# Optimization experiments

Hardware: AMD Instinct MI355X
Metric: run time of the kernel (lower is better)

## Reference

```python
import jax, jax.numpy as jnp
import numpy as np

C = 128
N, H, W = 4, 256, 256
BN_EPS = 1e-5


def _conv(x, w, b=None, groups=1):
    # x: [N,C,H,W], w: [O, I/groups, kh, kw]
    y = jax.lax.conv_general_dilated(
        x, w, window_strides=(1, 1), padding='SAME',
        dimension_numbers=('NCHW', 'OIHW', 'NCHW'),
        feature_group_count=groups)
    if b is not None:
        y = y + b[None, :, None, None]
    return y


def _bn(x, g, b, m, v):
    # eval-mode batchnorm with running stats
    inv = g / jnp.sqrt(v + BN_EPS)
    return x * inv[None, :, None, None] + (b - m * inv)[None, :, None, None]


def _patches3x3(x):
    # [N,C,H,W] -> [N,C,9,H,W], row-major kernel order (matches F.unfold)
    n, c, h, w = x.shape
    xp = jnp.pad(x, ((0, 0), (0, 0), (1, 1), (1, 1)))
    return jnp.stack([xp[:, :, i:i + h, j:j + w]
                      for i in range(3) for j in range(3)], axis=2)


def setup_inputs() -> dict:
    key = jax.random.key(0)
    ks = jax.random.split(key, 16)
    d = {}
    d['coef'] = jax.random.normal(ks[0], (N, C, H, W), jnp.float32)
    d['ms'] = jax.random.normal(ks[1], (N, C, H, W), jnp.float32)
    # fix_weight: depthwise 3x3, no bias + BN
    d['fix_w'] = jax.random.normal(ks[2], (C, 1, 3, 3), jnp.float32) * 0.1
    d['bn1_g'] = 1.0 + 0.1 * jax.random.normal(ks[3], (C,), jnp.float32)
    d['bn1_b'] = 0.1 * jax.random.normal(ks[4], (C,), jnp.float32)
    d['bn1_m'] = 0.1 * jax.random.normal(ks[5], (C,), jnp.float32)
    d['bn1_v'] = 0.5 + jax.random.uniform(ks[6], (C,), jnp.float32)
    # dyn_weight: Conv2d(C, 9, 3, pad 1)
    d['dyn_w'] = jax.random.normal(ks[7], (9, C, 3, 3), jnp.float32) * 0.05
    d['dyn_b'] = 0.05 * jax.random.normal(ks[8], (9,), jnp.float32)
    # dyn_tail BN
    d['bn2_g'] = 1.0 + 0.1 * jax.random.normal(ks[9], (C,), jnp.float32)
    d['bn2_b'] = 0.1 * jax.random.normal(ks[10], (C,), jnp.float32)
    d['bn2_m'] = 0.1 * jax.random.normal(ks[11], (C,), jnp.float32)
    d['bn2_v'] = 0.5 + jax.random.uniform(ks[12], (C,), jnp.float32)
    # refine 1x1: 2C -> C
    d['refine_w'] = jax.random.normal(ks[13], (C, 2 * C, 1, 1), jnp.float32) * 0.05
    d['refine_b'] = 0.05 * jax.random.normal(ks[14], (C,), jnp.float32)
    # SSModule joint_prob_head 3x3: C -> C
    d['joint_w'] = jax.random.normal(ks[15], (C, C, 3, 3), jnp.float32) * 0.03
    d['joint_b'] = 0.03 * jax.random.normal(jax.random.fold_in(key, 99), (C,), jnp.float32)
    return d


def reference(coef, ms, fix_w, bn1_g, bn1_b, bn1_m, bn1_v,
              dyn_w, dyn_b, bn2_g, bn2_b, bn2_m, bn2_v,
              refine_w, refine_b, joint_w, joint_b):
    # fix branch: depthwise conv + BN + ReLU
    fix_ms = jax.nn.relu(_bn(_conv(ms, fix_w, groups=C), bn1_g, bn1_b, bn1_m, bn1_v))
    # dynamic per-pixel kernel: [N,9,H,W], L1-normalized over kernel taps
    dyn_kernel = _conv(ms, dyn_w, dyn_b)
    dyn_kernel = dyn_kernel / jnp.sum(jnp.abs(dyn_kernel), axis=1, keepdims=True)
    # unfold + einsum: spatially-varying depthwise 3x3 conv
    patches = _patches3x3(ms)                                  # [N,C,9,H,W]
    dyn_ms = jnp.einsum('nkhw,nckhw->nchw', dyn_kernel, patches)
    dyn_ms = jax.nn.relu(_bn(dyn_ms, bn2_g, bn2_b, bn2_m, bn2_v))
    # concat + 1x1 refine
    fused = _conv(jnp.concatenate([dyn_ms, fix_ms], axis=1), refine_w, refine_b)
    # SSModule gating
    p = coef + fused
    p2 = jax.nn.sigmoid(_conv(p, joint_w, joint_b))
    return (1.0 - p2) * fused + p2 * coef
```

## Files before the change

kernel.cpp:

```cpp
#include <hip/hip_runtime.h>
#include <hip/hip_bf16.h>
#include <math.h>

#define N_ 4
#define C_ 128
#define H_ 256
#define W_ 256
#define HW_ (H_*W_)
#define BN_EPS 1e-5f

typedef __attribute__((ext_vector_type(8))) short bf16x8;
typedef __attribute__((ext_vector_type(4))) float floatx4;

__device__ __forceinline__ short f2bf(float v) {
    __hip_bfloat16 h = __float2bfloat16(v);
    return __builtin_bit_cast(short, h);
}

__global__ __launch_bounds__(256) void k_prep(const float* __restrict__ refine_w,
                                              const float* __restrict__ joint_w,
                                              short* __restrict__ rwf,
                                              short* __restrict__ jwf) {
    int i = blockIdx.x * 256 + threadIdx.x;
    if (i < 32768) {
        int j      = i & 7;
        int lane   = (i >> 3) & 63;
        int cotile = (i >> 9) & 7;
        int cic    = (i >> 12) & 7;
        int co = cotile * 16 + (lane & 15);
        int ii = cic * 32 + (lane >> 4) * 8 + j;
        rwf[i] = f2bf(refine_w[co * 256 + ii]);
    }
    if (i < 147456) {
        int j      = i & 7;
        int lane   = (i >> 3) & 63;
        int cotile = (i >> 9) & 7;
        int cic    = (i >> 12) & 3;
        int t      = i >> 14;
        int co = cotile * 16 + (lane & 15);
        int ci = cic * 32 + (lane >> 4) * 8 + j;
        jwf[i] = f2bf(joint_w[(co * 128 + ci) * 9 + t]);
    }
}

__global__ __launch_bounds__(256) void k_dyn(const float* __restrict__ ms,
                                             const float* __restrict__ dyn_w,
                                             const float* __restrict__ dyn_b,
                                             float* __restrict__ dk) {
    __shared__ float ms_s[8 * 18 * 18];
    int tid = threadIdx.x;
    int tx = tid & 15, ty = tid >> 4;
    int n = blockIdx.z;
    int h0 = blockIdx.y * 16, w0 = blockIdx.x * 16;
    float acc[9];
#pragma unroll
    for (int k = 0; k < 9; k++) acc[k] = dyn_b[k];

    for (int cc = 0; cc < 16; cc++) {
        __syncthreads();
        for (int e = tid; e < 8 * 18 * 18; e += 256) {
            int ch = e / 324, r = (e % 324) / 18, cl = e % 18;
            int gh = h0 + r - 1, gw = w0 + cl - 1;
            float v = 0.f;
            if (gh >= 0 && gh < H_ && gw >= 0 && gw < W_)
                v = ms[(size_t)(n * C_ + cc * 8 + ch) * HW_ + gh * W_ + gw];
            ms_s[e] = v;
        }
        __syncthreads();
        for (int c8 = 0; c8 < 8; c8++) {
            int c = cc * 8 + c8;
            float m[9];
#pragma unroll
            for (int dy = 0; dy < 3; dy++)
#pragma unroll
                for (int dx = 0; dx < 3; dx++)
                    m[dy * 3 + dx] = ms_s[c8 * 324 + (ty + dy) * 18 + tx + dx];
#pragma unroll
            for (int k = 0; k < 9; k++) {
#pragma unroll
                for (int t = 0; t < 9; t++)
                    acc[k] += m[t] * dyn_w[(k * C_ + c) * 9 + t];
            }
        }
    }
    float s = 0.f;
#pragma unroll
    for (int k = 0; k < 9; k++) s += fabsf(acc[k]);
    float inv = 1.f / s;
    int h = h0 + ty, w = w0 + tx;
#pragma unroll
    for (int k = 0; k < 9; k++)
        dk[(size_t)(n * 9 + k) * HW_ + h * W_ + w] = acc[k] * inv;
}

#define AIP 264
__global__ __launch_bounds__(256) void k_fused(const float* __restrict__ ms,
                                               const float* __restrict__ dk,
                                               const float* __restrict__ fix_w,
                                               const float* __restrict__ bn1_g,
                                               const float* __restrict__ bn1_b,
                                               const float* __restrict__ bn1_m,
                                               const float* __restrict__ bn1_v,
                                               const float* __restrict__ bn2_g,
                                               const float* __restrict__ bn2_b,
                                               const float* __restrict__ bn2_m,
                                               const float* __restrict__ bn2_v,
                                               const short* __restrict__ rwf,
                                               const float* __restrict__ refine_b,
                                               float* __restrict__ fused) {
    __shared__ short act_s[64 * AIP];
    __shared__ float ms_s[8 * 100];
    __shared__ float dk_s[9 * 64];
    int tid = threadIdx.x;
    int n = blockIdx.z;
    int h0 = blockIdx.y * 8, w0 = blockIdx.x * 8;

    for (int e = tid; e < 9 * 64; e += 256) {
        int t = e >> 6, px = e & 63;
        dk_s[e] = dk[(size_t)(n * 9 + t) * HW_ + (h0 + (px >> 3)) * W_ + (w0 + (px & 7))];
    }

    int c8 = tid & 7;
    int pxh = tid >> 3;

    for (int cc = 0; cc < 16; cc++) {
        __syncthreads();
        for (int e = tid; e < 800; e += 256) {
            int ch = e / 100, r = (e % 100) / 10, cl = e % 10;
            int gh = h0 + r - 1, gw = w0 + cl - 1;
            float v = 0.f;
            if (gh >= 0 && gh < H_ && gw >= 0 && gw < W_)
                v = ms[(size_t)(n * C_ + cc * 8 + ch) * HW_ + gh * W_ + gw];
            ms_s[e] = v;
        }
        __syncthreads();
        int c = cc * 8 + c8;
        float i1 = bn1_g[c] * rsqrtf(bn1_v[c] + BN_EPS);
        float b1 = bn1_b[c] - bn1_m[c] * i1;
        float i2 = bn2_g[c] * rsqrtf(bn2_v[c] + BN_EPS);
        float b2 = bn2_b[c] - bn2_m[c] * i2;
        float fw[9];
#pragma unroll
        for (int t = 0; t < 9; t++) fw[t] = fix_w[c * 9 + t];
#pragma unroll
        for (int it = 0; it < 2; it++) {
            int px = pxh + it * 32;
            int py = px >> 3, pxx = px & 7;
            float m[9];
#pragma unroll
            for (int dy = 0; dy < 3; dy++)
#pragma unroll
                for (int dx = 0; dx < 3; dx++)
                    m[dy * 3 + dx] = ms_s[c8 * 100 + (py + dy) * 10 + pxx + dx];
            float dyn = 0.f, fix = 0.f;
#pragma unroll
            for (int t = 0; t < 9; t++) {
                dyn += m[t] * dk_s[t * 64 + px];
                fix += m[t] * fw[t];
            }
            dyn = fmaxf(dyn * i2 + b2, 0.f);
            fix = fmaxf(fix * i1 + b1, 0.f);
            act_s[px * AIP + c] = f2bf(dyn);
            act_s[px * AIP + 128 + c] = f2bf(fix);
        }
    }
    __syncthreads();

    int lane = tid & 63;
    int wave = __builtin_amdgcn_readfirstlane(tid >> 6);
    int cl16 = lane & 15;
    int q = lane >> 4;
    int pxb = wave * 16;

    floatx4 acc[8];
#pragma unroll
    for (int ct = 0; ct < 8; ct++) acc[ct] = (floatx4){0.f, 0.f, 0.f, 0.f};

    const bf16x8* rwv = (const bf16x8*)rwf;
#pragma unroll
    for (int cic = 0; cic < 8; cic++) {
        bf16x8 B = *(const bf16x8*)(act_s + (pxb + cl16) * AIP + q * 8 + cic * 32);
        const bf16x8* Ap = rwv + cic * 8 * 64 + lane;
        bf16x8 A[8];
#pragma unroll
        for (int ct = 0; ct < 8; ct++) A[ct] = Ap[ct * 64];
#pragma unroll
        for (int ct = 0; ct < 8; ct++)
            acc[ct] = __builtin_amdgcn_mfma_f32_16x16x32_bf16(A[ct], B, acc[ct], 0, 0, 0);
    }

    int px = pxb + cl16;
    int h = h0 + (px >> 3), w = w0 + (px & 7);
#pragma unroll
    for (int ct = 0; ct < 8; ct++) {
#pragma unroll
        for (int r = 0; r < 4; r++) {
            int co = ct * 16 + q * 4 + r;
            fused[(size_t)(n * C_ + co) * HW_ + h * W_ + w] = acc[ct][r] + refine_b[co];
        }
    }
}

#define CIP 136
__global__ __launch_bounds__(256, 3) void k_out(const float* __restrict__ coef,
                                                const float* __restrict__ fused,
                                                const short* __restrict__ jwf,
                                                const float* __restrict__ joint_b,
                                                float* __restrict__ out) {
    __shared__ short p_s[180 * CIP];
    int tid = threadIdx.x;
    int n = blockIdx.z;
    int h0 = blockIdx.y * 8, w0 = blockIdx.x * 16;

    for (int it = 0; it < 90; it++) {
        int e = tid + it * 256;
        int ci = e / 180, sp = e - ci * 180;
        int row = sp / 18, col = sp - row * 18;
        int gh = h0 + row - 1, gw = w0 + col - 1;
        float v = 0.f;
        if (gh >= 0 && gh < H_ && gw >= 0 && gw < W_) {
            size_t idx = (size_t)(n * C_ + ci) * HW_ + gh * W_ + gw;
            v = coef[idx] + fused[idx];
        }
        p_s[sp * CIP + ci] = f2bf(v);
    }
    __syncthreads();

    int lane = tid & 63;
    int wave = __builtin_amdgcn_readfirstlane(tid >> 6);
    int c = lane & 15;
    int q = lane >> 4;
    int py0 = wave;
    int py1 = wave + 4;

    floatx4 acc[8][2];
#pragma unroll
    for (int ct = 0; ct < 8; ct++)
#pragma unroll
        for (int p = 0; p < 2; p++)
            acc[ct][p] = (floatx4){0.f, 0.f, 0.f, 0.f};

    const bf16x8* jwv = (const bf16x8*)jwf;

    for (int t = 0; t < 9; t++) {
        int dy = t / 3, dx = t - dy * 3;
        int sb0 = ((py0 + dy) * 18 + c + dx) * CIP + q * 8;
        int sb1 = ((py1 + dy) * 18 + c + dx) * CIP + q * 8;
#pragma unroll
        for (int cic = 0; cic < 4; cic++) {
            bf16x8 B0 = *(const bf16x8*)(p_s + sb0 + cic * 32);
            bf16x8 B1 = *(const bf16x8*)(p_s + sb1 + cic * 32);
            const bf16x8* Ap = jwv + ((t * 4 + cic) * 8) * 64 + lane;
            bf16x8 A[8];
#pragma unroll
            for (int ct = 0; ct < 8; ct++) A[ct] = Ap[ct * 64];
#pragma unroll
            for (int ct = 0; ct < 8; ct++) {
                acc[ct][0] = __builtin_amdgcn_mfma_f32_16x16x32_bf16(A[ct], B0, acc[ct][0], 0, 0, 0);
                acc[ct][1] = __builtin_amdgcn_mfma_f32_16x16x32_bf16(A[ct], B1, acc[ct][1], 0, 0, 0);
            }
        }
    }

    int w = w0 + c;
#pragma unroll
    for (int ct = 0; ct < 8; ct++) {
#pragma unroll
        for (int p = 0; p < 2; p++) {
            int h = h0 + (p == 0 ? py0 : py1);
#pragma unroll
            for (int r = 0; r < 4; r++) {
                int co = ct * 16 + q * 4 + r;
                size_t idx = (size_t)(n * C_ + co) * HW_ + h * W_ + w;
                float z = acc[ct][p][r] + joint_b[co];
                float p2 = 1.f / (1.f + __expf(-z));
                float f = fused[idx], cf = coef[idx];
                out[idx] = f + p2 * (cf - f);
            }
        }
    }
}

extern "C" void kernel_launch(void* const* d_in, const int* in_sizes, int n_in,
                              void* d_out, int out_size, void* d_ws, size_t ws_size,
                              hipStream_t stream) {
    const float* coef     = (const float*)d_in[0];
    const float* ms       = (const float*)d_in[1];
    const float* fix_w    = (const float*)d_in[2];
    const float* bn1_g    = (const float*)d_in[3];
    const float* bn1_b    = (const float*)d_in[4];
    const float* bn1_m    = (const float*)d_in[5];
    const float* bn1_v    = (const float*)d_in[6];
    const float* dyn_w    = (const float*)d_in[7];
    const float* dyn_b    = (const float*)d_in[8];
    const float* bn2_g    = (const float*)d_in[9];
    const float* bn2_b    = (const float*)d_in[10];
    const float* bn2_m    = (const float*)d_in[11];
    const float* bn2_v    = (const float*)d_in[12];
    const float* refine_w = (const float*)d_in[13];
    const float* refine_b = (const float*)d_in[14];
    const float* joint_w  = (const float*)d_in[15];
    const float* joint_b  = (const float*)d_in[16];
    float* out = (float*)d_out;

    float* ws    = (float*)d_ws;
    float* fused = ws;
    float* dk    = fused + (size_t)N_ * C_ * HW_;
    short* jwf   = (short*)(dk + (size_t)N_ * 9 * HW_);
    short* rwf   = jwf + 147456;

    dim3 blk(256);
    k_prep<<<dim3(576), blk, 0, stream>>>(refine_w, joint_w, rwf, jwf);
    k_dyn<<<dim3(16, 16, 4), blk, 0, stream>>>(ms, dyn_w, dyn_b, dk);
    k_fused<<<dim3(32, 32, 4), blk, 0, stream>>>(ms, dk, fix_w,
                                                 bn1_g, bn1_b, bn1_m, bn1_v,
                                                 bn2_g, bn2_b, bn2_m, bn2_v,
                                                 rwf, refine_b, fused);
    k_out<<<dim3(16, 32, 4), blk, 0, stream>>>(coef, fused, jwf, joint_b, out);
}
```

Baseline: 1.068 ms.

## Store fused and gate input as channel-last bf16 to cut k_out traffic

k_fused now writes fused and p = coef + fused as bf16 in an NHWC layout, replacing the fp32 NCHW fused buffer. The sum that k_out used to build in its staging loop now happens earlier, in k_fused. k_out loads the halo tile with 16-byte vector loads straight into LDS, dropping the strided per-channel coef+fused gathers and the per-element conversions. This lowers intermediate memory traffic, but rounding fused to bf16 adds error in the final blend, and k_fused must now also read coef.

```diff
diff --git a/kernel.cpp b/kernel.cpp
--- a/kernel.cpp
+++ b/kernel.cpp
@@ -15,6 +15,10 @@
 __device__ __forceinline__ short f2bf(float v) {
     __hip_bfloat16 h = __float2bfloat16(v);
     return __builtin_bit_cast(short, h);
+}
+__device__ __forceinline__ float bf2f(short s) {
+    unsigned u = ((unsigned)(unsigned short)s) << 16;
+    return __builtin_bit_cast(float, u);
 }
 
 __global__ __launch_bounds__(256) void k_prep(const float* __restrict__ refine_w,
@@ -96,6 +100,7 @@
 #define AIP 264
 __global__ __launch_bounds__(256) void k_fused(const float* __restrict__ ms,
                                                const float* __restrict__ dk,
+                                               const float* __restrict__ coef,
                                                const float* __restrict__ fix_w,
                                                const float* __restrict__ bn1_g,
                                                const float* __restrict__ bn1_b,
@@ -107,7 +112,8 @@
                                                const float* __restrict__ bn2_v,
                                                const short* __restrict__ rwf,
                                                const float* __restrict__ refine_b,
-                                               float* __restrict__ fused) {
+                                               short* __restrict__ fusedbf,
+                                               short* __restrict__ pbf) {
     __shared__ short act_s[64 * AIP];
     __shared__ float ms_s[8 * 100];
     __shared__ float dk_s[9 * 64];
@@ -191,19 +197,31 @@
 
     int px = pxb + cl16;
     int h = h0 + (px >> 3), w = w0 + (px & 7);
+    size_t spi = ((size_t)(n * H_) + h) * W_ + w;
 #pragma unroll
     for (int ct = 0; ct < 8; ct++) {
-#pragma unroll
-        for (int r = 0; r < 4; r++) {
-            int co = ct * 16 + q * 4 + r;
-            fused[(size_t)(n * C_ + co) * HW_ + h * W_ + w] = acc[ct][r] + refine_b[co];
-        }
+        int co0 = ct * 16 + q * 4;
+        float cf[4];
+#pragma unroll
+        for (int r = 0; r < 4; r++)
+            cf[r] = coef[(size_t)(n * C_ + co0 + r) * HW_ + h * W_ + w];
+        short4 fb, pb;
+        float f0 = acc[ct][0] + refine_b[co0 + 0];
+        float f1 = acc[ct][1] + refine_b[co0 + 1];
+        float f2_ = acc[ct][2] + refine_b[co0 + 2];
+        float f3 = acc[ct][3] + refine_b[co0 + 3];
+        fb.x = f2bf(f0);  fb.y = f2bf(f1);  fb.z = f2bf(f2_);  fb.w = f2bf(f3);
+        pb.x = f2bf(f0 + cf[0]); pb.y = f2bf(f1 + cf[1]);
+        pb.z = f2bf(f2_ + cf[2]); pb.w = f2bf(f3 + cf[3]);
+        *(short4*)(fusedbf + spi * 128 + co0) = fb;
+        *(short4*)(pbf + spi * 128 + co0) = pb;
     }
 }
 
 #define CIP 136
 __global__ __launch_bounds__(256, 3) void k_out(const float* __restrict__ coef,
-                                                const float* __restrict__ fused,
+                                                const short* __restrict__ fusedbf,
+                                                const short* __restrict__ pbf,
                                                 const short* __restrict__ jwf,
                                                 const float* __restrict__ joint_b,
                                                 float* __restrict__ out) {
@@ -212,17 +230,18 @@
     int n = blockIdx.z;
     int h0 = blockIdx.y * 8, w0 = blockIdx.x * 16;
 
-    for (int it = 0; it < 90; it++) {
-        int e = tid + it * 256;
-        int ci = e / 180, sp = e - ci * 180;
-        int row = sp / 18, col = sp - row * 18;
-        int gh = h0 + row - 1, gw = w0 + col - 1;
-        float v = 0.f;
-        if (gh >= 0 && gh < H_ && gw >= 0 && gw < W_) {
-            size_t idx = (size_t)(n * C_ + ci) * HW_ + gh * W_ + gw;
-            v = coef[idx] + fused[idx];
-        }
-        p_s[sp * CIP + ci] = f2bf(v);
+#pragma unroll
+    for (int it = 0; it < 12; it++) {
+        int e = it * 256 + tid;
+        if (e < 2880) {
+            int sp = e >> 4, g = e & 15;
+            int row = sp / 18, col = sp - row * 18;
+            int gh = h0 + row - 1, gw = w0 + col - 1;
+            uint4 v = {0u, 0u, 0u, 0u};
+            if (gh >= 0 && gh < H_ && gw >= 0 && gw < W_)
+                v = *(const uint4*)(pbf + (((size_t)n * H_ + gh) * W_ + gw) * 128 + g * 8);
+            *(uint4*)(p_s + sp * CIP + g * 8) = v;
+        }
     }
     __syncthreads();
 
@@ -264,17 +283,21 @@
 
     int w = w0 + c;
 #pragma unroll
-    for (int ct = 0; ct < 8; ct++) {
-#pragma unroll
-        for (int p = 0; p < 2; p++) {
-            int h = h0 + (p == 0 ? py0 : py1);
+    for (int p = 0; p < 2; p++) {
+        int h = h0 + (p == 0 ? py0 : py1);
+        size_t spi = ((size_t)(n * H_) + h) * W_ + w;
+#pragma unroll
+        for (int ct = 0; ct < 8; ct++) {
+            int co0 = ct * 16 + q * 4;
+            short4 fb = *(const short4*)(fusedbf + spi * 128 + co0);
+            float fv[4] = {bf2f(fb.x), bf2f(fb.y), bf2f(fb.z), bf2f(fb.w)};
 #pragma unroll
             for (int r = 0; r < 4; r++) {
-                int co = ct * 16 + q * 4 + r;
+                int co = co0 + r;
                 size_t idx = (size_t)(n * C_ + co) * HW_ + h * W_ + w;
                 float z = acc[ct][p][r] + joint_b[co];
                 float p2 = 1.f / (1.f + __expf(-z));
-                float f = fused[idx], cf = coef[idx];
+                float f = fv[r], cf = coef[idx];
                 out[idx] = f + p2 * (cf - f);
             }
         }
@@ -303,18 +326,18 @@
     const float* joint_b  = (const float*)d_in[16];
     float* out = (float*)d_out;
 
-    float* ws    = (float*)d_ws;
-    float* fused = ws;
-    float* dk    = fused + (size_t)N_ * C_ * HW_;
-    short* jwf   = (short*)(dk + (size_t)N_ * 9 * HW_);
-    short* rwf   = jwf + 147456;
+    short* fusedbf = (short*)d_ws;
+    short* pbf     = fusedbf + (size_t)N_ * C_ * HW_;
+    float* dk      = (float*)(pbf + (size_t)N_ * C_ * HW_);
+    short* jwf     = (short*)(dk + (size_t)N_ * 9 * HW_);
+    short* rwf     = jwf + 147456;
 
     dim3 blk(256);
     k_prep<<<dim3(576), blk, 0, stream>>>(refine_w, joint_w, rwf, jwf);
     k_dyn<<<dim3(16, 16, 4), blk, 0, stream>>>(ms, dyn_w, dyn_b, dk);
-    k_fused<<<dim3(32, 32, 4), blk, 0, stream>>>(ms, dk, fix_w,
+    k_fused<<<dim3(32, 32, 4), blk, 0, stream>>>(ms, dk, coef, fix_w,
                                                  bn1_g, bn1_b, bn1_m, bn1_v,
                                                  bn2_g, bn2_b, bn2_m, bn2_v,
-                                                 rwf, refine_b, fused);
-    k_out<<<dim3(16, 32, 4), blk, 0, stream>>>(coef, fused, jwf, joint_b, out);
-}
+                                                 rwf, refine_b, fusedbf, pbf);
+    k_out<<<dim3(16, 32, 4), blk, 0, stream>>>(coef, fusedbf, pbf, jwf, joint_b, out);
+}
```

Result: faster. 1.015 ms (-4.9%).
